# Kernel tuning notes

Hardware: AMD Instinct MI355X
Metric: run time of the kernel (lower is better)

Reference implementation:

```python
import jax, jax.numpy as jnp
import numpy as np
from jax import lax

N_BLOCK = 4  # unfold kernel/stride

SOBEL_X = jnp.array([[-1., 0., 1.], [-2., 0., 2.], [-1., 0., 1.]], dtype=jnp.float32)
SOBEL_Y = jnp.array([[-1., -2., -1.], [0., 0., 0.], [1., 2., 1.]], dtype=jnp.float32)


def setup_inputs() -> dict:
    key = jax.random.key(0)
    k1, k2 = jax.random.split(key)
    output = jax.random.normal(k1, (16, 1, 1024, 1024), dtype=jnp.float32)
    target = jax.random.normal(k2, (16, 1, 1024, 1024), dtype=jnp.float32)
    return {"output": output, "target": target}


def _sobel(img, kernel):
    # img: (B,1,H,W); cross-correlation with padding 1 (matches nn.Conv2d)
    return lax.conv_general_dilated(img, kernel[None, None], (1, 1), ((1, 1), (1, 1)))


def _block_var(g, n):
    # g: (B,1,H,W) -> per non-overlapping n x n block variance (unbiased=False)
    B, _, H, W = g.shape
    blocks = g.reshape(B, H // n, n, W // n, n)
    m = blocks.mean(axis=(2, 4))
    m2 = (blocks * blocks).mean(axis=(2, 4))
    return (m2 - m * m).reshape(B, -1)  # (B, (H//n)*(W//n))


def reference(output, target):
    loss = jnp.float32(0.0)
    for kern in (SOBEL_X, SOBEL_Y):
        var_out = _block_var(_sobel(output, kern), N_BLOCK)
        var_tgt = _block_var(_sobel(target, kern), N_BLOCK)
        d = var_out - var_tgt
        loss = loss + jnp.sum(d * d)  # MSELoss(reduction='sum')
    return loss
```

## Files before the change

kernel.cpp:

```cpp
#include <hip/hip_runtime.h>

#define IMG_H 1024
#define IMG_W 1024


struct Row { float4 qa0, qa1, qb0, qb1; float ea, eb; };

__global__ __launch_bounds__(256) void gvl_main(const float* __restrict__ A,
                                                const float* __restrict__ B,
                                                float* __restrict__ partial) {
    const int t    = threadIdx.x;
    const int wave = (blockIdx.x << 2) | (t >> 6);
    const int lane = t & 63;
    const int img   = wave >> 8;
    const int rem   = wave & 255;
    const int band  = rem >> 1;
    const int strip = rem & 1;
    const int y0    = band << 3;
    const int c0    = (strip << 9) | (lane << 3);
    const int ecol  = strip ? 511 : 512;

    const float* __restrict__ Ab = A + (size_t)img * (size_t)(IMG_H * IMG_W);
    const float* __restrict__ Bb = B + (size_t)img * (size_t)(IMG_H * IMG_W);

    const float eLs = strip ? 1.f : 0.f;
    const float eRs = strip ? 0.f : 1.f;
    const float maskPrev = (band > 0)    ? 1.f : 0.f;
    const float zlast    = (band == 127) ? 0.f : 1.f;

    auto load_row = [&](int y, Row& R) {
        int yc = y < 0 ? 0 : (y > IMG_H - 1 ? IMG_H - 1 : y);
        const float* ra = Ab + (size_t)yc * IMG_W;
        const float* rb = Bb + (size_t)yc * IMG_W;
        R.qa0 = *reinterpret_cast<const float4*>(ra + c0);
        R.qa1 = *reinterpret_cast<const float4*>(ra + c0 + 4);
        R.qb0 = *reinterpret_cast<const float4*>(rb + c0);
        R.qb1 = *reinterpret_cast<const float4*>(rb + c0 + 4);
        R.ea  = ra[ecol];
        R.eb  = rb[ecol];
    };

    float aX2[8], aX1[8], aB2[8], aB1[8];
    float bX2[8], bX1[8], bB2[8], bB1[8];
    float sX[2][2], sXX[2][2], sY[2][2], sYY[2][2];
#pragma unroll
    for (int i = 0; i < 2; ++i)
#pragma unroll
        for (int j = 0; j < 2; ++j) { sX[i][j] = sXX[i][j] = sY[i][j] = sYY[i][j] = 0.f; }

    auto calc_h = [&](const float4 q0, const float4 q1, float e, float m,
                      float (&hX)[8], float (&hB)[8]) {
        float lv = __shfl_up(q1.w, 1);
        float rv = __shfl_down(q0.x, 1);
        lv = (lane == 0)  ? e * eLs : lv;
        rv = (lane == 63) ? e * eRs : rv;
        float w[10] = {lv, q0.x, q0.y, q0.z, q0.w, q1.x, q1.y, q1.z, q1.w, rv};
#pragma unroll
        for (int c = 0; c < 8; ++c) {
            hX[c] = (w[c + 2] - w[c]) * m;
            hB[c] = (w[c] + 2.f * w[c + 1] + w[c + 2]) * m;
        }
    };

    auto proc_img = [&](const float4 q0, const float4 q1, float e, float m,
                        float (&X2)[8], float (&X1)[8], float (&B2)[8], float (&B1)[8],
                        float (&sXi)[2], float (&sXXi)[2],
                        float (&sYi)[2], float (&sYYi)[2]) {
        float lv = __shfl_up(q1.w, 1);
        float rv = __shfl_down(q0.x, 1);
        lv = (lane == 0)  ? e * eLs : lv;
        rv = (lane == 63) ? e * eRs : rv;
        float w[10] = {lv, q0.x, q0.y, q0.z, q0.w, q1.x, q1.y, q1.z, q1.w, rv};
#pragma unroll
        for (int c = 0; c < 8; ++c) {
            float hX = (w[c + 2] - w[c]) * m;
            float hB = (w[c] + 2.f * w[c + 1] + w[c + 2]) * m;
            float gx = X2[c] + 2.f * X1[c] + hX;
            float gy = hB - B2[c];
            const int blk = c >> 2;
            sXi[blk] += gx;  sXXi[blk] += gx * gx;
            sYi[blk] += gy;  sYYi[blk] += gy * gy;
            X2[c] = X1[c];  X1[c] = hX;
            B2[c] = B1[c];  B1[c] = hB;
        }
    };

    float loss = 0.f;
    auto finalize = [&]() {
#pragma unroll
        for (int j = 0; j < 2; ++j) {
            float mXa = sX[0][j] * 0.0625f, mYa = sY[0][j] * 0.0625f;
            float vXa = sXX[0][j] * 0.0625f - mXa * mXa;
            float vYa = sYY[0][j] * 0.0625f - mYa * mYa;
            float mXb = sX[1][j] * 0.0625f, mYb = sY[1][j] * 0.0625f;
            float vXb = sXX[1][j] * 0.0625f - mXb * mXb;
            float vYb = sYY[1][j] * 0.0625f - mYb * mYb;
            float dX = vXa - vXb, dY = vYa - vYb;
            loss += dX * dX + dY * dY;
#pragma unroll
            for (int i = 0; i < 2; ++i) { sX[i][j] = sXX[i][j] = sY[i][j] = sYY[i][j] = 0.f; }
        }
    };

    Row Rm, R0, Rb0, Rb1;
    load_row(y0 - 1, Rm);
    load_row(y0,     R0);
    load_row(y0 + 1, Rb0);
    calc_h(Rm.qa0, Rm.qa1, Rm.ea, maskPrev, aX2, aB2);
    calc_h(Rm.qb0, Rm.qb1, Rm.eb, maskPrev, bX2, bB2);
    calc_h(R0.qa0, R0.qa1, R0.ea, 1.f, aX1, aB1);
    calc_h(R0.qb0, R0.qb1, R0.eb, 1.f, bX1, bB1);

#pragma unroll
    for (int k = 0; k < 8; ++k) {
        Row& cur = (k & 1) ? Rb1 : Rb0;
        Row& nxt = (k & 1) ? Rb0 : Rb1;
        if (k < 7) load_row(y0 + 2 + k, nxt);
        const float m = (k == 7) ? zlast : 1.f;
        proc_img(cur.qa0, cur.qa1, cur.ea, m, aX2, aX1, aB2, aB1,
                 sX[0], sXX[0], sY[0], sYY[0]);
        proc_img(cur.qb0, cur.qb1, cur.eb, m, bX2, bX1, bB2, bB1,
                 sX[1], sXX[1], sY[1], sYY[1]);
        if ((k & 3) == 3) finalize();
    }

#pragma unroll
    for (int off = 32; off > 0; off >>= 1) loss += __shfl_down(loss, off);
    if (lane == 0) partial[wave] = loss;
}

__global__ __launch_bounds__(256) void gvl_final(const float* __restrict__ partial,
                                                 float* __restrict__ out) {
    int t = threadIdx.x;
    float s = 0.f;
#pragma unroll
    for (int i = 0; i < 16; ++i) s += partial[t + (i << 8)];
#pragma unroll
    for (int off = 32; off > 0; off >>= 1) s += __shfl_down(s, off);
    __shared__ float ws[4];
    if ((t & 63) == 0) ws[t >> 6] = s;
    __syncthreads();
    if (t == 0) out[0] = ws[0] + ws[1] + ws[2] + ws[3];
}

extern "C" void kernel_launch(void* const* d_in, const int* in_sizes, int n_in,
                              void* d_out, int out_size, void* d_ws, size_t ws_size,
                              hipStream_t stream) {
    const float* out_img = (const float*)d_in[0];
    const float* tgt_img = (const float*)d_in[1];
    float* partial = (float*)d_ws;
    gvl_main<<<1024, 256, 0, stream>>>(out_img, tgt_img, partial);
    gvl_final<<<1, 256, 0, stream>>>(partial, (float*)d_out);
}
```

Baseline: 31.23 us.

## Deepen row prefetch with inline-asm loads and explicit vmcnt waits, taller bands

Each wave now processes a 16-row band instead of 8, which halves the grid and lowers the halo-row overhead. Rows go through a 4-deep ring buffer filled by inline-asm global_load_dwordx4/x2 instructions, and explicit s_waitcnt vmcnt counts keep three rows in flight while the current one is computed. The edge-column loads become a single dwordx2, and launch bounds add a 2-blocks-per-CU hint. The hand-tuned waitcnt counts depend on exactly six loads per row and on the compiler not reordering around the sched barriers; fewer waves may also reduce latency hiding.

```diff
diff --git a/kernel.cpp b/kernel.cpp
--- a/kernel.cpp
+++ b/kernel.cpp
@@ -4,86 +4,66 @@
 #define IMG_W 1024
 
 
-struct Row { float4 qa0, qa1, qb0, qb1; float ea, eb; };
+struct Row { float4 a0, a1, b0, b1; float2 ea, eb; };
 
-__global__ __launch_bounds__(256) void gvl_main(const float* __restrict__ A,
-                                                const float* __restrict__ B,
-                                                float* __restrict__ partial) {
+__device__ __forceinline__ float4 gload4(const float* p) {
+    float4 d;
+    asm volatile("global_load_dwordx4 %0, %1, off" : "=v"(d) : "v"(p));
+    return d;
+}
+__device__ __forceinline__ float2 gload2(const float* p) {
+    float2 d;
+    asm volatile("global_load_dwordx2 %0, %1, off" : "=v"(d) : "v"(p));
+    return d;
+}
+template <int N> __device__ __forceinline__ void waitv() {
+    if constexpr (N >= 3)      asm volatile("s_waitcnt vmcnt(18)" ::: "memory");
+    else if constexpr (N == 2) asm volatile("s_waitcnt vmcnt(12)" ::: "memory");
+    else if constexpr (N == 1) asm volatile("s_waitcnt vmcnt(6)" ::: "memory");
+    else                       asm volatile("s_waitcnt vmcnt(0)" ::: "memory");
+    __builtin_amdgcn_sched_barrier(0);
+}
+
+__global__ __launch_bounds__(256, 2) void gvl_main(const float* __restrict__ A,
+                                                   const float* __restrict__ B,
+                                                   float* __restrict__ partial) {
     const int t    = threadIdx.x;
     const int wave = (blockIdx.x << 2) | (t >> 6);
     const int lane = t & 63;
-    const int img   = wave >> 8;
-    const int rem   = wave & 255;
+    const int img   = wave >> 7;
+    const int rem   = wave & 127;
     const int band  = rem >> 1;
     const int strip = rem & 1;
-    const int y0    = band << 3;
+    const int y0    = band << 4;
     const int c0    = (strip << 9) | (lane << 3);
-    const int ecol  = strip ? 511 : 512;
 
     const float* __restrict__ Ab = A + (size_t)img * (size_t)(IMG_H * IMG_W);
     const float* __restrict__ Bb = B + (size_t)img * (size_t)(IMG_H * IMG_W);
 
-    const float eLs = strip ? 1.f : 0.f;
-    const float eRs = strip ? 0.f : 1.f;
-    const float maskPrev = (band > 0)    ? 1.f : 0.f;
-    const float zlast    = (band == 127) ? 0.f : 1.f;
+    const float m0  = (band == 0)  ? 0.f : 1.f;
+    const float m17 = (band == 63) ? 0.f : 1.f;
+    const bool  s1  = (strip == 1);
 
-    auto load_row = [&](int y, Row& R) {
+    Row Rb[4];
+    auto issue_row = [&](int i, Row& R) {
+        int y  = y0 - 1 + i;
         int yc = y < 0 ? 0 : (y > IMG_H - 1 ? IMG_H - 1 : y);
-        const float* ra = Ab + (size_t)yc * IMG_W;
-        const float* rb = Bb + (size_t)yc * IMG_W;
-        R.qa0 = *reinterpret_cast<const float4*>(ra + c0);
-        R.qa1 = *reinterpret_cast<const float4*>(ra + c0 + 4);
-        R.qb0 = *reinterpret_cast<const float4*>(rb + c0);
-        R.qb1 = *reinterpret_cast<const float4*>(rb + c0 + 4);
-        R.ea  = ra[ecol];
-        R.eb  = rb[ecol];
+        const float* ra = Ab + ((size_t)yc << 10);
+        const float* rb = Bb + ((size_t)yc << 10);
+        R.a0 = gload4(ra + c0);
+        R.a1 = gload4(ra + c0 + 4);
+        R.b0 = gload4(rb + c0);
+        R.b1 = gload4(rb + c0 + 4);
+        R.ea = gload2(ra + 511);
+        R.eb = gload2(rb + 511);
     };
 
-    float aX2[8], aX1[8], aB2[8], aB1[8];
-    float bX2[8], bX1[8], bB2[8], bB1[8];
+    float hX2[2][8], hX1[2][8], hB2[2][8], hB1[2][8];
     float sX[2][2], sXX[2][2], sY[2][2], sYY[2][2];
 #pragma unroll
     for (int i = 0; i < 2; ++i)
 #pragma unroll
         for (int j = 0; j < 2; ++j) { sX[i][j] = sXX[i][j] = sY[i][j] = sYY[i][j] = 0.f; }
-
-    auto calc_h = [&](const float4 q0, const float4 q1, float e, float m,
-                      float (&hX)[8], float (&hB)[8]) {
-        float lv = __shfl_up(q1.w, 1);
-        float rv = __shfl_down(q0.x, 1);
-        lv = (lane == 0)  ? e * eLs : lv;
-        rv = (lane == 63) ? e * eRs : rv;
-        float w[10] = {lv, q0.x, q0.y, q0.z, q0.w, q1.x, q1.y, q1.z, q1.w, rv};
-#pragma unroll
-        for (int c = 0; c < 8; ++c) {
-            hX[c] = (w[c + 2] - w[c]) * m;
-            hB[c] = (w[c] + 2.f * w[c + 1] + w[c + 2]) * m;
-        }
-    };
-
-    auto proc_img = [&](const float4 q0, const float4 q1, float e, float m,
-                        float (&X2)[8], float (&X1)[8], float (&B2)[8], float (&B1)[8],
-                        float (&sXi)[2], float (&sXXi)[2],
-                        float (&sYi)[2], float (&sYYi)[2]) {
-        float lv = __shfl_up(q1.w, 1);
-        float rv = __shfl_down(q0.x, 1);
-        lv = (lane == 0)  ? e * eLs : lv;
-        rv = (lane == 63) ? e * eRs : rv;
-        float w[10] = {lv, q0.x, q0.y, q0.z, q0.w, q1.x, q1.y, q1.z, q1.w, rv};
-#pragma unroll
-        for (int c = 0; c < 8; ++c) {
-            float hX = (w[c + 2] - w[c]) * m;
-            float hB = (w[c] + 2.f * w[c + 1] + w[c + 2]) * m;
-            float gx = X2[c] + 2.f * X1[c] + hX;
-            float gy = hB - B2[c];
-            const int blk = c >> 2;
-            sXi[blk] += gx;  sXXi[blk] += gx * gx;
-            sYi[blk] += gy;  sYYi[blk] += gy * gy;
-            X2[c] = X1[c];  X1[c] = hX;
-            B2[c] = B1[c];  B1[c] = hB;
-        }
-    };
 
     float loss = 0.f;
     auto finalize = [&]() {
@@ -102,26 +82,49 @@
         }
     };
 
-    Row Rm, R0, Rb0, Rb1;
-    load_row(y0 - 1, Rm);
-    load_row(y0,     R0);
-    load_row(y0 + 1, Rb0);
-    calc_h(Rm.qa0, Rm.qa1, Rm.ea, maskPrev, aX2, aB2);
-    calc_h(Rm.qb0, Rm.qb1, Rm.eb, maskPrev, bX2, bB2);
-    calc_h(R0.qa0, R0.qa1, R0.ea, 1.f, aX1, aB1);
-    calc_h(R0.qb0, R0.qb1, R0.eb, 1.f, bX1, bB1);
+    auto consume_img = [&](int im, const float4 q0, const float4 q1,
+                           const float2 e, float m, bool emit) {
+        float lvr = __shfl_up(q1.w, 1);
+        float rvr = __shfl_down(q0.x, 1);
+        float eL = s1 ? e.x : 0.f;
+        float eR = s1 ? 0.f : e.y;
+        float lv = (lane == 0)  ? eL : lvr;
+        float rv = (lane == 63) ? eR : rvr;
+        float w[10] = {lv, q0.x, q0.y, q0.z, q0.w, q1.x, q1.y, q1.z, q1.w, rv};
+#pragma unroll
+        for (int c = 0; c < 8; ++c) {
+            float hX0 = (w[c + 2] - w[c]) * m;
+            float hB0 = (w[c] + 2.f * w[c + 1] + w[c + 2]) * m;
+            if (emit) {
+                float gx = hX2[im][c] + 2.f * hX1[im][c] + hX0;
+                float gy = hB0 - hB2[im][c];
+                const int blk = c >> 2;
+                sX[im][blk]  += gx;  sXX[im][blk] += gx * gx;
+                sY[im][blk]  += gy;  sYY[im][blk] += gy * gy;
+            }
+            hX2[im][c] = hX1[im][c];  hX1[im][c] = hX0;
+            hB2[im][c] = hB1[im][c];  hB1[im][c] = hB0;
+        }
+    };
+
+    issue_row(0, Rb[0]);
+    issue_row(1, Rb[1]);
+    issue_row(2, Rb[2]);
 
 #pragma unroll
-    for (int k = 0; k < 8; ++k) {
-        Row& cur = (k & 1) ? Rb1 : Rb0;
-        Row& nxt = (k & 1) ? Rb0 : Rb1;
-        if (k < 7) load_row(y0 + 2 + k, nxt);
-        const float m = (k == 7) ? zlast : 1.f;
-        proc_img(cur.qa0, cur.qa1, cur.ea, m, aX2, aX1, aB2, aB1,
-                 sX[0], sXX[0], sY[0], sYY[0]);
-        proc_img(cur.qb0, cur.qb1, cur.eb, m, bX2, bX1, bB2, bB1,
-                 sX[1], sXX[1], sY[1], sYY[1]);
-        if ((k & 3) == 3) finalize();
+    for (int i = 0; i < 18; ++i) {
+        if (i + 3 < 18) issue_row(i + 3, Rb[(i + 3) & 3]);
+        const int ahead = (i + 3 <= 17) ? 3 : (17 - i);
+        if (ahead == 3)      waitv<3>();
+        else if (ahead == 2) waitv<2>();
+        else if (ahead == 1) waitv<1>();
+        else                 waitv<0>();
+        Row& R = Rb[i & 3];
+        const float m = (i == 0) ? m0 : ((i == 17) ? m17 : 1.f);
+        const bool emit = (i >= 2);
+        consume_img(0, R.a0, R.a1, R.ea, m, emit);
+        consume_img(1, R.b0, R.b1, R.eb, m, emit);
+        if (i >= 5 && ((i - 5) & 3) == 0) finalize();
     }
 
 #pragma unroll
@@ -134,7 +137,7 @@
     int t = threadIdx.x;
     float s = 0.f;
 #pragma unroll
-    for (int i = 0; i < 16; ++i) s += partial[t + (i << 8)];
+    for (int i = 0; i < 8; ++i) s += partial[t + (i << 8)];
 #pragma unroll
     for (int off = 32; off > 0; off >>= 1) s += __shfl_down(s, off);
     __shared__ float ws[4];
@@ -149,6 +152,6 @@
     const float* out_img = (const float*)d_in[0];
     const float* tgt_img = (const float*)d_in[1];
     float* partial = (float*)d_ws;
-    gvl_main<<<1024, 256, 0, stream>>>(out_img, tgt_img, partial);
+    gvl_main<<<512, 256, 0, stream>>>(out_img, tgt_img, partial);
     gvl_final<<<1, 256, 0, stream>>>(partial, (float*)d_out);
 }
```

Measured after the change: 29.52 us. -5.5%, faster.
